# Performance work log

Measured on AMD Instinct MI355X. Metric: run time of the kernel, lower is better.

The kernel has to match this reference:

```python
import jax, jax.numpy as jnp
import numpy as np

H = 12        # heads
D = 768       # d_model
DK = D // H   # per-head dim
B, S = 1, 4096


def setup_inputs() -> dict:
    key = jax.random.key(0)
    ks = jax.random.split(key, 8)
    scale = 1.0 / np.sqrt(D)
    return {
        "q": jax.random.normal(ks[0], (B, S, D), jnp.float32),
        "k": jax.random.normal(ks[1], (B, S, D), jnp.float32),
        "v": jax.random.normal(ks[2], (B, S, D), jnp.float32),
        "Wq": jax.random.normal(ks[3], (D, D), jnp.float32) * scale,
        "bq": jnp.zeros((D,), jnp.float32),
        "Wk": jax.random.normal(ks[4], (D, D), jnp.float32) * scale,
        "bk": jnp.zeros((D,), jnp.float32),
        "Wv": jax.random.normal(ks[5], (D, D), jnp.float32) * scale,
        "bv": jnp.zeros((D,), jnp.float32),
        "Wo": jax.random.normal(ks[6], (D, D), jnp.float32) * scale,
        "bo": jnp.zeros((D,), jnp.float32),
    }


def reference(q, k, v, Wq, bq, Wk, bk, Wv, bv, Wo, bo):
    bs, sq, _ = q.shape
    sk = k.shape[1]
    # projections, then split heads: (b, h, s, dk)
    qh = (q @ Wq + bq).reshape(bs, sq, H, DK).transpose(0, 2, 1, 3)
    kh = (k @ Wk + bk).reshape(bs, sk, H, DK).transpose(0, 2, 1, 3)
    vh = (v @ Wv + bv).reshape(bs, sk, H, DK).transpose(0, 2, 1, 3)
    # scaled dot-product attention (mask=None, dropout inactive)
    scores = jnp.einsum("bhqd,bhkd->bhqk", qh, kh) / jnp.sqrt(jnp.float32(DK))
    attn = jax.nn.softmax(scores, axis=-1)
    ctx = jnp.einsum("bhqk,bhkd->bhqd", attn, vh)
    concat = ctx.transpose(0, 2, 1, 3).reshape(bs, sq, D)
    return concat @ Wo + bo
```

## Files before the change

### kernel.cpp

```cpp
#include <hip/hip_runtime.h>
#include <hip/hip_bf16.h>


constexpr int S_LEN = 4096;
constexpr int D_MODEL = 768;
constexpr int N_HEADS = 12;
constexpr int D_HEAD = 64;
constexpr int SEG = 2;
constexpr int SEG_LEN = S_LEN / SEG;

#define QSCALE 0.180336880111120f

typedef _Float16 f16;
typedef __attribute__((ext_vector_type(8))) _Float16 f16x8;
typedef __attribute__((ext_vector_type(4))) _Float16 f16x4;
typedef __attribute__((ext_vector_type(4))) float f32x4;

__global__ __launch_bounds__(256) void prep_kernel(
    const float* __restrict__ q, const float* __restrict__ k,
    const float* __restrict__ v, f16* __restrict__ qh,
    f16* __restrict__ kh, f16* __restrict__ vh,
    const float* __restrict__ W0, const float* __restrict__ W1,
    const float* __restrict__ W2, const float* __restrict__ W3,
    f16* __restrict__ WtBase)
{
    __shared__ float T[64][65];
    int bid = blockIdx.x;
    const int t = threadIdx.x;
    if (bid < 4608) {
        int g = bid / 1536, r = bid % 1536;
        const float* x = (g == 0) ? q : (g == 1) ? k : v;
        f16* y = (g == 0) ? qh : (g == 1) ? kh : vh;
        int i = (r * 256 + t) * 8;
        float4 a = *(const float4*)&x[i];
        float4 b = *(const float4*)&x[i + 4];
        f16x8 h = { (f16)a.x, (f16)a.y, (f16)a.z, (f16)a.w,
                    (f16)b.x, (f16)b.y, (f16)b.z, (f16)b.w };
        *(f16x8*)&y[i] = h;
        return;
    }
    bid -= 4608;
    int g = bid / 144, r = bid % 144;
    const float* W = (g == 0) ? W0 : (g == 1) ? W1 : (g == 2) ? W2 : W3;
    f16* Wt = WtBase + (size_t)g * D_MODEL * D_MODEL;
    const int r0 = (r / 12) * 64;
    const int c0 = (r % 12) * 64;
    #pragma unroll
    for (int i = 0; i < 16; ++i) {
        int e = t + 256 * i; int rr = e >> 6, cc = e & 63;
        T[rr][cc] = W[(size_t)(r0 + rr) * D_MODEL + c0 + cc];
    }
    __syncthreads();
    #pragma unroll
    for (int i = 0; i < 16; ++i) {
        int e = t + 256 * i; int rr = e >> 6, cc = e & 63;
        Wt[(size_t)(c0 + rr) * D_MODEL + r0 + cc] = (f16)T[cc][rr];
    }
}

#define GSTR 72

__device__ __forceinline__ void gemm128_core(
    const f16* __restrict__ A, const f16* __restrict__ B,
    f16* As, f16* Bs, int K, int row0, int col0, int t, f32x4 acc[4][4])
{
    const int w = t >> 6, l = t & 63, quad = l >> 4, l15 = l & 15;
    const int wm = (w & 1) * 64, wn = (w >> 1) * 64;

    for (int k0 = 0; k0 < K; k0 += 64) {
        __syncthreads();
        #pragma unroll
        for (int i = 0; i < 4; ++i) {
            int idx = i * 256 + t;
            int r = idx >> 3, c = (idx & 7) * 8;
            *(f16x8*)&As[r * GSTR + c] =
                *(const f16x8*)&A[(size_t)(row0 + r) * K + k0 + c];
            *(f16x8*)&Bs[r * GSTR + c] =
                *(const f16x8*)&B[(size_t)(col0 + r) * K + k0 + c];
        }
        __syncthreads();

        #pragma unroll
        for (int kc = 0; kc < 2; ++kc) {
            f16x8 af[4], bf[4];
            #pragma unroll
            for (int mt = 0; mt < 4; ++mt)
                af[mt] = *(f16x8*)&As[(wm + mt * 16 + l15) * GSTR + kc * 32 + quad * 8];
            #pragma unroll
            for (int nt = 0; nt < 4; ++nt)
                bf[nt] = *(f16x8*)&Bs[(wn + nt * 16 + l15) * GSTR + kc * 32 + quad * 8];
            #pragma unroll
            for (int mt = 0; mt < 4; ++mt)
                #pragma unroll
                for (int nt = 0; nt < 4; ++nt)
                    acc[mt][nt] = __builtin_amdgcn_mfma_f32_16x16x32_f16(
                        af[mt], bf[nt], acc[mt][nt], 0, 0, 0);
        }
    }
}

__global__ __launch_bounds__(256) void qkv_gemm_kernel(
    const f16* __restrict__ qh, const f16* __restrict__ kh,
    const f16* __restrict__ vh, const f16* __restrict__ WtBase,
    const float* __restrict__ bq, const float* __restrict__ bk,
    const float* __restrict__ bv,
    f16* __restrict__ Qp, f16* __restrict__ Kp, f16* __restrict__ Vpt)
{
    __shared__ f16 As[128 * GSTR];
    __shared__ f16 Bs[128 * GSTR];
    const size_t DD = (size_t)D_MODEL * D_MODEL;
    int bid = blockIdx.x;
    int g = bid / 192, r = bid % 192;

    const f16 *A, *B; const float* bias; f16* Y;
    int N; bool biasRow; float scale;
    int row0, col0;
    if (g == 0) {
        A = qh; B = WtBase; bias = bq; Y = Qp;
        N = D_MODEL; biasRow = false; scale = QSCALE;
        row0 = (r / 6) * 128; col0 = (r % 6) * 128;
    } else if (g == 1) {
        A = kh; B = WtBase + DD; bias = bk; Y = Kp;
        N = D_MODEL; biasRow = false; scale = 1.0f;
        row0 = (r / 6) * 128; col0 = (r % 6) * 128;
    } else {
        A = WtBase + 2 * DD; B = vh; bias = bv; Y = Vpt;
        N = S_LEN; biasRow = true; scale = 1.0f;
        row0 = (r / 32) * 128; col0 = (r % 32) * 128;
    }

    f32x4 acc[4][4];
    #pragma unroll
    for (int i = 0; i < 4; ++i)
        #pragma unroll
        for (int j = 0; j < 4; ++j) acc[i][j] = (f32x4){0.f, 0.f, 0.f, 0.f};

    const int t = threadIdx.x;
    gemm128_core(A, B, As, Bs, D_MODEL, row0, col0, t, acc);

    const int w = t >> 6, l = t & 63, quad = l >> 4, l15 = l & 15;
    const int wm = (w & 1) * 64, wn = (w >> 1) * 64;
    #pragma unroll
    for (int mt = 0; mt < 4; ++mt) {
        #pragma unroll
        for (int nt = 0; nt < 4; ++nt) {
            int col = col0 + wn + nt * 16 + l15;
            #pragma unroll
            for (int reg = 0; reg < 4; ++reg) {
                int row = row0 + wm + mt * 16 + quad * 4 + reg;
                float b = biasRow ? bias[row] : bias[col];
                Y[(size_t)row * N + col] = (f16)((acc[mt][nt][reg] + b) * scale);
            }
        }
    }
}

#define LSTR 72

__global__ __launch_bounds__(256, 4) void flash_attn_part_kernel(
    const f16* __restrict__ Q, const f16* __restrict__ K,
    const f16* __restrict__ Vg, f16* __restrict__ Opart,
    float* __restrict__ lsum)
{
    __shared__ f16 Ks[64 * LSTR];
    __shared__ f16 Vt[64 * LSTR];
    __shared__ f16 Ps[128 * LSTR];

    const int t    = threadIdx.x;
    const int w    = t >> 6;
    const int l    = t & 63;
    const int quad = l >> 4;
    const int l15  = l & 15;
    const int h    = blockIdx.y;
    const int q0   = blockIdx.x * 128;
    const int seg  = blockIdx.z;
    const int c0   = h * D_HEAD;
    const size_t SD = (size_t)S_LEN * D_MODEL;

    f16x8 qa[2][2];
    #pragma unroll
    for (int qt = 0; qt < 2; ++qt) {
        const f16* qrow = Q + (size_t)(q0 + w * 32 + qt * 16 + l15) * D_MODEL + c0;
        qa[qt][0] = *(const f16x8*)&qrow[quad * 8];
        qa[qt][1] = *(const f16x8*)&qrow[32 + quad * 8];
    }

    f32x4 ctx[2][4];
    float lAcc[2] = {0.f, 0.f};
    #pragma unroll
    for (int qt = 0; qt < 2; ++qt)
        #pragma unroll
        for (int i = 0; i < 4; ++i) ctx[qt][i] = (f32x4){0.f, 0.f, 0.f, 0.f};

    const int kt0 = seg * SEG_LEN;
    for (int kt = kt0; kt < kt0 + SEG_LEN; kt += 64) {
        __syncthreads();
        #pragma unroll
        for (int i = 0; i < 2; ++i) {
            int idx = i * 256 + t;
            int r = idx >> 3, c = (idx & 7) * 8;
            *(f16x8*)&Ks[r * LSTR + c] =
                *(const f16x8*)&K[(size_t)(kt + r) * D_MODEL + c0 + c];
            *(f16x8*)&Vt[r * LSTR + c] =
                *(const f16x8*)&Vg[(size_t)(c0 + r) * S_LEN + kt + c];
        }
        __syncthreads();

        #pragma unroll
        for (int nt = 0; nt < 4; ++nt) {
            f16x8 kb0 = *(f16x8*)&Ks[(nt * 16 + l15) * LSTR + quad * 8];
            f16x8 kb1 = *(f16x8*)&Ks[(nt * 16 + l15) * LSTR + 32 + quad * 8];
            #pragma unroll
            for (int qt = 0; qt < 2; ++qt) {
                f32x4 z = (f32x4){0.f, 0.f, 0.f, 0.f};
                z = __builtin_amdgcn_mfma_f32_16x16x32_f16(kb0, qa[qt][0], z, 0, 0, 0);
                z = __builtin_amdgcn_mfma_f32_16x16x32_f16(kb1, qa[qt][1], z, 0, 0, 0);
                float p0 = __builtin_amdgcn_exp2f(z[0]);
                float p1 = __builtin_amdgcn_exp2f(z[1]);
                float p2 = __builtin_amdgcn_exp2f(z[2]);
                float p3 = __builtin_amdgcn_exp2f(z[3]);
                lAcc[qt] += (p0 + p1) + (p2 + p3);
                f16x4 pk = { (f16)p0, (f16)p1, (f16)p2, (f16)p3 };
                *(f16x4*)&Ps[(w * 32 + qt * 16 + l15) * LSTR + nt * 16 + quad * 4] = pk;
            }
        }

        f16x8 pa[2][2];
        #pragma unroll
        for (int qt = 0; qt < 2; ++qt)
            #pragma unroll
            for (int kc = 0; kc < 2; ++kc)
                pa[qt][kc] = *(f16x8*)&Ps[(w * 32 + qt * 16 + l15) * LSTR + kc * 32 + quad * 8];
        #pragma unroll
        for (int mt = 0; mt < 4; ++mt) {
            f16x8 vb0 = *(f16x8*)&Vt[(mt * 16 + l15) * LSTR + quad * 8];
            f16x8 vb1 = *(f16x8*)&Vt[(mt * 16 + l15) * LSTR + 32 + quad * 8];
            #pragma unroll
            for (int qt = 0; qt < 2; ++qt) {
                ctx[qt][mt] = __builtin_amdgcn_mfma_f32_16x16x32_f16(vb0, pa[qt][0], ctx[qt][mt], 0, 0, 0);
                ctx[qt][mt] = __builtin_amdgcn_mfma_f32_16x16x32_f16(vb1, pa[qt][1], ctx[qt][mt], 0, 0, 0);
            }
        }
    }

    #pragma unroll
    for (int qt = 0; qt < 2; ++qt) {
        int qrow = q0 + w * 32 + qt * 16 + l15;
        #pragma unroll
        for (int mt = 0; mt < 4; ++mt) {
            f16x4 ov = { (f16)ctx[qt][mt][0], (f16)ctx[qt][mt][1],
                         (f16)ctx[qt][mt][2], (f16)ctx[qt][mt][3] };
            *(f16x4*)&Opart[(size_t)seg * SD + (size_t)qrow * D_MODEL
                            + c0 + mt * 16 + quad * 4] = ov;
        }
        float s = lAcc[qt];
        s += __shfl_xor(s, 16);
        s += __shfl_xor(s, 32);
        if (quad == 0)
            lsum[((size_t)seg * N_HEADS + h) * S_LEN + qrow] = s;
    }
}

__global__ __launch_bounds__(256) void combine_kernel(
    const f16* __restrict__ Opart, const float* __restrict__ lsum,
    f16* __restrict__ Ctx)
{
    const size_t SD = (size_t)S_LEN * D_MODEL;
    int tid = blockIdx.x * 256 + threadIdx.x;
    int idx = tid * 8;
    int row = idx / D_MODEL;
    int c   = idx % D_MODEL;
    int h   = c >> 6;
    float l0 = lsum[(size_t)h * S_LEN + row];
    float l1 = lsum[((size_t)N_HEADS + h) * S_LEN + row];
    float inv = 1.0f / (l0 + l1);
    f16x8 o0 = *(const f16x8*)&Opart[(size_t)row * D_MODEL + c];
    f16x8 o1 = *(const f16x8*)&Opart[SD + (size_t)row * D_MODEL + c];
    f16x8 r;
    #pragma unroll
    for (int j = 0; j < 8; ++j)
        r[j] = (f16)(((float)o0[j] + (float)o1[j]) * inv);
    *(f16x8*)&Ctx[(size_t)row * D_MODEL + c] = r;
}

__global__ __launch_bounds__(256) void oproj_kernel(
    const f16* __restrict__ Ctx, const f16* __restrict__ Wto,
    const float* __restrict__ bo, float* __restrict__ out)
{
    __shared__ f16 As[128 * GSTR];
    __shared__ f16 Bs[128 * GSTR];
    int bid = blockIdx.x;
    int row0 = (bid / 6) * 128, col0 = (bid % 6) * 128;

    f32x4 acc[4][4];
    #pragma unroll
    for (int i = 0; i < 4; ++i)
        #pragma unroll
        for (int j = 0; j < 4; ++j) acc[i][j] = (f32x4){0.f, 0.f, 0.f, 0.f};

    const int t = threadIdx.x;
    gemm128_core(Ctx, Wto, As, Bs, D_MODEL, row0, col0, t, acc);

    const int w = t >> 6, l = t & 63, quad = l >> 4, l15 = l & 15;
    const int wm = (w & 1) * 64, wn = (w >> 1) * 64;
    #pragma unroll
    for (int mt = 0; mt < 4; ++mt) {
        #pragma unroll
        for (int nt = 0; nt < 4; ++nt) {
            int col = col0 + wn + nt * 16 + l15;
            float b = bo[col];
            #pragma unroll
            for (int reg = 0; reg < 4; ++reg) {
                int row = row0 + wm + mt * 16 + quad * 4 + reg;
                out[(size_t)row * D_MODEL + col] = acc[mt][nt][reg] + b;
            }
        }
    }
}

extern "C" void kernel_launch(void* const* d_in, const int* in_sizes, int n_in,
                              void* d_out, int out_size, void* d_ws, size_t ws_size,
                              hipStream_t stream)
{
    const float* q  = (const float*)d_in[0];
    const float* k  = (const float*)d_in[1];
    const float* v  = (const float*)d_in[2];
    const float* Wq = (const float*)d_in[3];
    const float* bq = (const float*)d_in[4];
    const float* Wk = (const float*)d_in[5];
    const float* bk = (const float*)d_in[6];
    const float* Wv = (const float*)d_in[7];
    const float* bv = (const float*)d_in[8];
    const float* Wo = (const float*)d_in[9];
    const float* bo = (const float*)d_in[10];
    float* out = (float*)d_out;

    const size_t SD = (size_t)S_LEN * D_MODEL;
    const size_t DD = (size_t)D_MODEL * D_MODEL;
    f16* base   = (f16*)d_ws;
    f16* WtBase = base;
    f16* Wto    = WtBase + 3 * DD;
    f16* Qp     = base + 4 * DD;
    f16* Kp     = Qp + SD;
    f16* Vpt    = Kp + SD;
    f16* qh     = Vpt + SD;
    f16* kh     = qh + SD;
    f16* vh     = kh + SD;
    f16* Opart  = qh;
    f16* Ctx    = qh + 2 * SD;
    float* lsum = (float*)(base + 4 * DD + 6 * SD);

    prep_kernel<<<3 * 1536 + 4 * 144, 256, 0, stream>>>(
        q, k, v, qh, kh, vh, Wq, Wk, Wv, Wo, WtBase);

    qkv_gemm_kernel<<<3 * 192, 256, 0, stream>>>(
        qh, kh, vh, WtBase, bq, bk, bv, Qp, Kp, Vpt);

    dim3 gAttn(S_LEN / 128, N_HEADS, SEG);
    flash_attn_part_kernel<<<gAttn, 256, 0, stream>>>(Qp, Kp, Vpt, Opart, lsum);

    combine_kernel<<<1536, 256, 0, stream>>>(Opart, lsum, Ctx);

    oproj_kernel<<<192, 256, 0, stream>>>(Ctx, Wto, bo, out);
}
```

Before: 246.4 us.

## Prefetch next tiles into registers and keep P fragments in registers

Both the GEMM core and the flash-attention kernel now load the next K-tile from global memory into registers while the current tile is being computed, so global-load latency overlaps with MFMA work. The attention kernel also stops staging the probability matrix through shared memory. It keeps the exp'd scores as f16x4 register fragments and feeds them straight into 16x16x16 MFMAs against V, which removes an LDS round trip and the shared buffer. The cost is more registers for the prefetch buffers and fragments, which can lower occupancy. It also replaces half as many 16x16x32 MFMAs with twice as many 16x16x16 ones.

```diff
diff --git a/kernel.cpp b/kernel.cpp
--- a/kernel.cpp
+++ b/kernel.cpp
@@ -67,18 +67,36 @@
     const int w = t >> 6, l = t & 63, quad = l >> 4, l15 = l & 15;
     const int wm = (w & 1) * 64, wn = (w >> 1) * 64;
 
+    f16x8 pa[4], pb[4];
+    #pragma unroll
+    for (int i = 0; i < 4; ++i) {
+        int idx = i * 256 + t;
+        int r = idx >> 3, c = (idx & 7) * 8;
+        pa[i] = *(const f16x8*)&A[(size_t)(row0 + r) * K + c];
+        pb[i] = *(const f16x8*)&B[(size_t)(col0 + r) * K + c];
+    }
+
     for (int k0 = 0; k0 < K; k0 += 64) {
         __syncthreads();
         #pragma unroll
         for (int i = 0; i < 4; ++i) {
             int idx = i * 256 + t;
             int r = idx >> 3, c = (idx & 7) * 8;
-            *(f16x8*)&As[r * GSTR + c] =
-                *(const f16x8*)&A[(size_t)(row0 + r) * K + k0 + c];
-            *(f16x8*)&Bs[r * GSTR + c] =
-                *(const f16x8*)&B[(size_t)(col0 + r) * K + k0 + c];
+            *(f16x8*)&As[r * GSTR + c] = pa[i];
+            *(f16x8*)&Bs[r * GSTR + c] = pb[i];
         }
         __syncthreads();
+
+        int kn = k0 + 64;
+        if (kn < K) {
+            #pragma unroll
+            for (int i = 0; i < 4; ++i) {
+                int idx = i * 256 + t;
+                int r = idx >> 3, c = (idx & 7) * 8;
+                pa[i] = *(const f16x8*)&A[(size_t)(row0 + r) * K + kn + c];
+                pb[i] = *(const f16x8*)&B[(size_t)(col0 + r) * K + kn + c];
+            }
+        }
 
         #pragma unroll
         for (int kc = 0; kc < 2; ++kc) {
@@ -164,7 +182,6 @@
 {
     __shared__ f16 Ks[64 * LSTR];
     __shared__ f16 Vt[64 * LSTR];
-    __shared__ f16 Ps[128 * LSTR];
 
     const int t    = threadIdx.x;
     const int w    = t >> 6;
@@ -193,19 +210,39 @@
         for (int i = 0; i < 4; ++i) ctx[qt][i] = (f32x4){0.f, 0.f, 0.f, 0.f};
 
     const int kt0 = seg * SEG_LEN;
+
+    f16x8 kreg[2], vreg[2];
+    #pragma unroll
+    for (int i = 0; i < 2; ++i) {
+        int idx = i * 256 + t;
+        int r = idx >> 3, c = (idx & 7) * 8;
+        kreg[i] = *(const f16x8*)&K[(size_t)(kt0 + r) * D_MODEL + c0 + c];
+        vreg[i] = *(const f16x8*)&Vg[(size_t)(c0 + r) * S_LEN + kt0 + c];
+    }
+
     for (int kt = kt0; kt < kt0 + SEG_LEN; kt += 64) {
         __syncthreads();
         #pragma unroll
         for (int i = 0; i < 2; ++i) {
             int idx = i * 256 + t;
             int r = idx >> 3, c = (idx & 7) * 8;
-            *(f16x8*)&Ks[r * LSTR + c] =
-                *(const f16x8*)&K[(size_t)(kt + r) * D_MODEL + c0 + c];
-            *(f16x8*)&Vt[r * LSTR + c] =
-                *(const f16x8*)&Vg[(size_t)(c0 + r) * S_LEN + kt + c];
+            *(f16x8*)&Ks[r * LSTR + c] = kreg[i];
+            *(f16x8*)&Vt[r * LSTR + c] = vreg[i];
         }
         __syncthreads();
 
+        int ktn = kt + 64;
+        if (ktn < kt0 + SEG_LEN) {
+            #pragma unroll
+            for (int i = 0; i < 2; ++i) {
+                int idx = i * 256 + t;
+                int r = idx >> 3, c = (idx & 7) * 8;
+                kreg[i] = *(const f16x8*)&K[(size_t)(ktn + r) * D_MODEL + c0 + c];
+                vreg[i] = *(const f16x8*)&Vg[(size_t)(c0 + r) * S_LEN + ktn + c];
+            }
+        }
+
+        f16x4 pfrag[2][4];
         #pragma unroll
         for (int nt = 0; nt < 4; ++nt) {
             f16x8 kb0 = *(f16x8*)&Ks[(nt * 16 + l15) * LSTR + quad * 8];
@@ -220,25 +257,19 @@
                 float p2 = __builtin_amdgcn_exp2f(z[2]);
                 float p3 = __builtin_amdgcn_exp2f(z[3]);
                 lAcc[qt] += (p0 + p1) + (p2 + p3);
-                f16x4 pk = { (f16)p0, (f16)p1, (f16)p2, (f16)p3 };
-                *(f16x4*)&Ps[(w * 32 + qt * 16 + l15) * LSTR + nt * 16 + quad * 4] = pk;
-            }
-        }
-
-        f16x8 pa[2][2];
-        #pragma unroll
-        for (int qt = 0; qt < 2; ++qt)
-            #pragma unroll
-            for (int kc = 0; kc < 2; ++kc)
-                pa[qt][kc] = *(f16x8*)&Ps[(w * 32 + qt * 16 + l15) * LSTR + kc * 32 + quad * 8];
+                pfrag[qt][nt] = (f16x4){ (f16)p0, (f16)p1, (f16)p2, (f16)p3 };
+            }
+        }
+
         #pragma unroll
         for (int mt = 0; mt < 4; ++mt) {
-            f16x8 vb0 = *(f16x8*)&Vt[(mt * 16 + l15) * LSTR + quad * 8];
-            f16x8 vb1 = *(f16x8*)&Vt[(mt * 16 + l15) * LSTR + 32 + quad * 8];
-            #pragma unroll
-            for (int qt = 0; qt < 2; ++qt) {
-                ctx[qt][mt] = __builtin_amdgcn_mfma_f32_16x16x32_f16(vb0, pa[qt][0], ctx[qt][mt], 0, 0, 0);
-                ctx[qt][mt] = __builtin_amdgcn_mfma_f32_16x16x32_f16(vb1, pa[qt][1], ctx[qt][mt], 0, 0, 0);
+            #pragma unroll
+            for (int nt = 0; nt < 4; ++nt) {
+                f16x4 va = *(f16x4*)&Vt[(mt * 16 + l15) * LSTR + nt * 16 + quad * 4];
+                #pragma unroll
+                for (int qt = 0; qt < 2; ++qt)
+                    ctx[qt][mt] = __builtin_amdgcn_mfma_f32_16x16x16f16(
+                        va, pfrag[qt][nt], ctx[qt][mt], 0, 0, 0);
             }
         }
     }
```

Result: faster. 224.7 us (-8.8%).
